# Optimization experiments

Hardware: AMD Instinct MI355X
Metric: run time of the kernel (lower is better)

The kernel has to match this reference:

```python
import jax, jax.numpy as jnp
import numpy as np

VOCAB, B, T, H, E = 32000, 32, 128, 128, 128

def setup_inputs() -> dict:
    key = jax.random.key(0)
    ks = jax.random.split(key, 10)
    s = 0.05
    return {
        "inputs": jax.random.randint(ks[0], (B, T), 0, VOCAB, dtype=jnp.int32),
        "emb": jax.random.normal(ks[1], (VOCAB, E), jnp.float32) * s,
        "W0": jax.random.normal(ks[2], (E, 4 * H), jnp.float32) * s,
        "U0": jax.random.normal(ks[3], (H, 4 * H), jnp.float32) * s,
        "b0": jnp.zeros((4 * H,), jnp.float32),
        "W1": jax.random.normal(ks[4], (H, 4 * H), jnp.float32) * s,
        "U1": jax.random.normal(ks[5], (H, 4 * H), jnp.float32) * s,
        "b1": jnp.zeros((4 * H,), jnp.float32),
        "Wd": jax.random.normal(ks[6], (H, VOCAB), jnp.float32) * s,
        "bd": jnp.zeros((VOCAB,), jnp.float32),
    }

def _lstm_cell(x, h, c, W, U, b):
    # Keras LSTMCell gate order: i, f, c(candidate), o
    z = x @ W + h @ U + b  # [B, 4H]
    zi, zf, zc, zo = jnp.split(z, 4, axis=-1)
    i = jax.nn.sigmoid(zi)
    f = jax.nn.sigmoid(zf)
    o = jax.nn.sigmoid(zo)
    c_new = f * c + i * jnp.tanh(zc)
    h_new = o * jnp.tanh(c_new)
    return h_new, c_new

def reference(inputs, emb, W0, U0, b0, W1, U1, b1, Wd, bd):
    x = emb[inputs]  # [B, T, E]
    xt = jnp.transpose(x, (1, 0, 2))  # [T, B, E]
    zeros = jnp.zeros((x.shape[0], H), x.dtype)
    init = (zeros, zeros, zeros, zeros)  # h0, c0, h1, c1

    def step(carry, x_t):
        h0, c0, h1, c1 = carry
        h0, c0 = _lstm_cell(x_t, h0, c0, W0, U0, b0)
        h1, c1 = _lstm_cell(h0, h1, c1, W1, U1, b1)
        return (h0, c0, h1, c1), h1

    _, ys = jax.lax.scan(step, init, xt)  # ys: [T, B, H]
    y = jnp.transpose(ys, (1, 0, 2))  # [B, T, H]
    logits = y @ Wd + bd  # [B, T, VOCAB]
    return logits
```

## Files before the change

kernel.cpp:

```cpp
#include <hip/hip_runtime.h>
#include <math.h>

#define BB 32
#define TT 128
#define EE 128
#define HD 128
#define G4 512
#define NV 32000

typedef _Float16 f16x2  __attribute__((ext_vector_type(2)));
typedef _Float16 f16x4v __attribute__((ext_vector_type(4)));
typedef _Float16 f16x8  __attribute__((ext_vector_type(8)));
typedef float    f32x4  __attribute__((ext_vector_type(4)));

__global__ __launch_bounds__(256) void k_embed(
    const int* __restrict__ inputs, const float* __restrict__ emb,
    const float* __restrict__ W0, const float* __restrict__ b0,
    float* __restrict__ Z0x)
{
    __shared__ float xs[8][EE];
    const int r0 = blockIdx.x * 8;
    const int tid = threadIdx.x;
    for (int i = tid; i < 8 * EE; i += 256) {
        int r = i >> 7, e = i & 127;
        int tok = inputs[r0 + r];
        xs[r][e] = emb[tok * EE + e];
    }
    __syncthreads();
    const int c2 = tid * 2;
    float2 bb2 = *(const float2*)&b0[c2];
    float acc[8][2];
    #pragma unroll
    for (int r = 0; r < 8; ++r) { acc[r][0] = bb2.x; acc[r][1] = bb2.y; }
    for (int e = 0; e < EE; ++e) {
        float2 w = *(const float2*)&W0[e * G4 + c2];
        #pragma unroll
        for (int r = 0; r < 8; ++r) {
            float x = xs[r][e];
            acc[r][0] = fmaf(x, w.x, acc[r][0]);
            acc[r][1] = fmaf(x, w.y, acc[r][1]);
        }
    }
    #pragma unroll
    for (int r = 0; r < 8; ++r) {
        float2 o2; o2.x = acc[r][0]; o2.y = acc[r][1];
        *(float2*)&Z0x[(size_t)(r0 + r) * G4 + c2] = o2;
    }
}

__device__ __forceinline__ float sigf(float x) {
    return __builtin_amdgcn_rcpf(1.f + __builtin_amdgcn_exp2f(x * -1.44269504088896f));
}
__device__ __forceinline__ float tanh_f(float x) {
    return 1.f - 2.f * __builtin_amdgcn_rcpf(1.f + __builtin_amdgcn_exp2f(x * 2.88539008177793f));
}
__device__ __forceinline__ f16x8 ldfrag(const float* __restrict__ M, int col, int k0) {
    f16x8 v;
    #pragma unroll
    for (int j = 0; j < 8; ++j) v[j] = (_Float16)M[(size_t)(k0 + j) * G4 + col];
    return v;
}

#define REP8(X) X(0) X(1) X(2) X(3) X(4) X(5) X(6) X(7)
#define MFMA(acc, a, b) acc = __builtin_amdgcn_mfma_f32_16x16x32_f16(a, b, acc, 0, 0, 0)

#define DECLF(n) f16x8 u0_##n##_0, u0_##n##_1, u0_##n##_2, u0_##n##_3, \
                       w1_##n##_0, w1_##n##_1, w1_##n##_2, w1_##n##_3, \
                       u1_##n##_0, u1_##n##_1, u1_##n##_2, u1_##n##_3;

#define LOADF(n) { const int cn = wc0 + (n) * 16 + lo16; \
    u0_##n##_0 = ldfrag(U0, cn, khi);      u0_##n##_1 = ldfrag(U0, cn, 32 + khi); \
    u0_##n##_2 = ldfrag(U0, cn, 64 + khi); u0_##n##_3 = ldfrag(U0, cn, 96 + khi); \
    w1_##n##_0 = ldfrag(W1, cn, khi);      w1_##n##_1 = ldfrag(W1, cn, 32 + khi); \
    w1_##n##_2 = ldfrag(W1, cn, 64 + khi); w1_##n##_3 = ldfrag(W1, cn, 96 + khi); \
    asm("" : "+a"(w1_##n##_0), "+a"(w1_##n##_1), "+a"(w1_##n##_2), "+a"(w1_##n##_3)); \
    u1_##n##_0 = ldfrag(U1, cn, khi);      u1_##n##_1 = ldfrag(U1, cn, 32 + khi); \
    u1_##n##_2 = ldfrag(U1, cn, 64 + khi); u1_##n##_3 = ldfrag(U1, cn, 96 + khi); \
    asm("" : "+a"(u1_##n##_0), "+a"(u1_##n##_1), "+a"(u1_##n##_2), "+a"(u1_##n##_3)); }

#define PA(n) { f32x4 acc = {0.f, 0.f, 0.f, 0.f}; \
    MFMA(acc, ha0, u0_##n##_0); MFMA(acc, ha1, u0_##n##_1); \
    MFMA(acc, ha2, u0_##n##_2); MFMA(acc, ha3, u0_##n##_3); \
    if (lane < 32) { const int cw = wc0 + (n) * 16 + lo16; const int br = (lane >> 4) * 4; \
        zbuf[br + 0][cw] = acc[0]; zbuf[br + 1][cw] = acc[1]; \
        zbuf[br + 2][cw] = acc[2]; zbuf[br + 3][cw] = acc[3]; } }

#define PC(n) { f32x4 acc = {0.f, 0.f, 0.f, 0.f}; \
    MFMA(acc, ha0, w1_##n##_0); MFMA(acc, ha1, w1_##n##_1); \
    MFMA(acc, ha2, w1_##n##_2); MFMA(acc, ha3, w1_##n##_3); \
    MFMA(acc, hb0, u1_##n##_0); MFMA(acc, hb1, u1_##n##_1); \
    MFMA(acc, hb2, u1_##n##_2); MFMA(acc, hb3, u1_##n##_3); \
    if (lane < 32) { const int cw = wc0 + (n) * 16 + lo16; const int br = (lane >> 4) * 4; \
        zbuf[br + 0][cw] = acc[0]; zbuf[br + 1][cw] = acc[1]; \
        zbuf[br + 2][cw] = acc[2]; zbuf[br + 3][cw] = acc[3]; } }

#define GT0(K, ZI, ZF, ZC, ZO) { \
    float ig = sigf(ZI), fg = sigf(ZF), og = sigf(ZO), gg = tanh_f(ZC); \
    float cn = fg * c0v[K] + ig * gg; c0v[K] = cn; hv[K] = (_Float16)(og * tanh_f(cn)); }

#define GT1(K, ZI, ZF, ZC, ZO, YO) { \
    float ig = sigf(ZI), fg = sigf(ZF), og = sigf(ZO), gg = tanh_f(ZC); \
    float cn = fg * c1v[K] + ig * gg; c1v[K] = cn; float hn = og * tanh_f(cn); \
    hv[K] = (_Float16)hn; YO = hn; }

__global__ __launch_bounds__(256, 1) void k_lstm_mw(
    const float* __restrict__ Z0x,
    const float* __restrict__ U0, const float* __restrict__ W1,
    const float* __restrict__ U1, const float* __restrict__ b1,
    float* __restrict__ y,
    const float* __restrict__ Wd, _Float16* __restrict__ Whi, _Float16* __restrict__ Wlo)
{
    const int tid  = threadIdx.x;

    if (blockIdx.x >= 4) {
        if (Whi == nullptr) return;
        const int g = (blockIdx.x - 4) * 256 + tid;
        const int chunk = g >> 6;
        const int ln = g & 63;
        const int ntile = chunk >> 2;
        const int kstep = chunk & 3;
        const int n = ntile * 16 + (ln & 15);
        const int kb = kstep * 32 + (ln >> 4) * 8;
        _Float16 hi[8], lo[8];
        #pragma unroll
        for (int j = 0; j < 8; ++j) {
            float v = Wd[(size_t)(kb + j) * NV + n];
            hi[j] = (_Float16)v;
            lo[j] = (_Float16)(v - (float)hi[j]);
        }
        *(float4*)&Whi[(size_t)chunk * 512 + ln * 8] = *(const float4*)hi;
        *(float4*)&Wlo[(size_t)chunk * 512 + ln * 8] = *(const float4*)lo;
        return;
    }

    const int lane = tid & 63;
    const int wc0  = (tid >> 6) * 128;
    const int lo16 = lane & 15;
    const int khi  = (lane >> 4) * 8;
    const int B0   = blockIdx.x * 8;

    __shared__ float     zbuf[8][516];
    __shared__ _Float16  h0p[16][136];
    __shared__ _Float16  h1p[16][136];

    REP8(DECLF)
    REP8(LOADF)

    const int bq  = tid >> 5;
    const int h0i = (tid & 31) * 4;
    const float* zx_base = Z0x + ((size_t)(B0 + bq) * TT) * G4;
    float*       y_base  = y   + ((size_t)(B0 + bq) * TT) * HD + h0i;

    const float4 b1_i = *(const float4*)&b1[0 * 128 + h0i];
    const float4 b1_f = *(const float4*)&b1[1 * 128 + h0i];
    const float4 b1_c = *(const float4*)&b1[2 * 128 + h0i];
    const float4 b1_o = *(const float4*)&b1[3 * 128 + h0i];

    for (int i = tid; i < 16 * 136; i += 256) {
        ((_Float16*)h0p)[i] = (_Float16)0.f;
        ((_Float16*)h1p)[i] = (_Float16)0.f;
    }
    f32x4 c0v = {0.f, 0.f, 0.f, 0.f};
    f32x4 c1v = {0.f, 0.f, 0.f, 0.f};
    __syncthreads();

    for (int t = 0; t < TT; ++t) {
        const float* zx = zx_base + (size_t)t * G4;
        const float4 x_i = *(const float4*)&zx[0 * 128 + h0i];
        const float4 x_f = *(const float4*)&zx[1 * 128 + h0i];
        const float4 x_c = *(const float4*)&zx[2 * 128 + h0i];
        const float4 x_o = *(const float4*)&zx[3 * 128 + h0i];

        {
            f16x8 ha0 = *(const f16x8*)&h0p[lo16][khi];
            f16x8 ha1 = *(const f16x8*)&h0p[lo16][32 + khi];
            f16x8 ha2 = *(const f16x8*)&h0p[lo16][64 + khi];
            f16x8 ha3 = *(const f16x8*)&h0p[lo16][96 + khi];
            REP8(PA)
        }
        __syncthreads();

        {
            const float4 zi4 = *(const float4*)&zbuf[bq][0 * 128 + h0i];
            const float4 zf4 = *(const float4*)&zbuf[bq][1 * 128 + h0i];
            const float4 zc4 = *(const float4*)&zbuf[bq][2 * 128 + h0i];
            const float4 zo4 = *(const float4*)&zbuf[bq][3 * 128 + h0i];
            f16x4v hv;
            GT0(0, zi4.x + x_i.x, zf4.x + x_f.x, zc4.x + x_c.x, zo4.x + x_o.x)
            GT0(1, zi4.y + x_i.y, zf4.y + x_f.y, zc4.y + x_c.y, zo4.y + x_o.y)
            GT0(2, zi4.z + x_i.z, zf4.z + x_f.z, zc4.z + x_c.z, zo4.z + x_o.z)
            GT0(3, zi4.w + x_i.w, zf4.w + x_f.w, zc4.w + x_c.w, zo4.w + x_o.w)
            *(f16x4v*)&h0p[bq][h0i] = hv;
        }
        __syncthreads();

        {
            f16x8 ha0 = *(const f16x8*)&h0p[lo16][khi];
            f16x8 ha1 = *(const f16x8*)&h0p[lo16][32 + khi];
            f16x8 ha2 = *(const f16x8*)&h0p[lo16][64 + khi];
            f16x8 ha3 = *(const f16x8*)&h0p[lo16][96 + khi];
            f16x8 hb0 = *(const f16x8*)&h1p[lo16][khi];
            f16x8 hb1 = *(const f16x8*)&h1p[lo16][32 + khi];
            f16x8 hb2 = *(const f16x8*)&h1p[lo16][64 + khi];
            f16x8 hb3 = *(const f16x8*)&h1p[lo16][96 + khi];
            REP8(PC)
        }
        __syncthreads();

        {
            const float4 zi4 = *(const float4*)&zbuf[bq][0 * 128 + h0i];
            const float4 zf4 = *(const float4*)&zbuf[bq][1 * 128 + h0i];
            const float4 zc4 = *(const float4*)&zbuf[bq][2 * 128 + h0i];
            const float4 zo4 = *(const float4*)&zbuf[bq][3 * 128 + h0i];
            f16x4v hv; float4 yv;
            GT1(0, zi4.x + b1_i.x, zf4.x + b1_f.x, zc4.x + b1_c.x, zo4.x + b1_o.x, yv.x)
            GT1(1, zi4.y + b1_i.y, zf4.y + b1_f.y, zc4.y + b1_c.y, zo4.y + b1_o.y, yv.y)
            GT1(2, zi4.z + b1_i.z, zf4.z + b1_f.z, zc4.z + b1_c.z, zo4.z + b1_o.z, yv.z)
            GT1(3, zi4.w + b1_i.w, zf4.w + b1_f.w, zc4.w + b1_c.w, zo4.w + b1_o.w, yv.w)
            *(f16x4v*)&h1p[bq][h0i] = hv;
            *(float4*)(y_base + (size_t)t * HD) = yv;
        }
        __syncthreads();
    }
}

__global__ __launch_bounds__(256) void k_ysplit(
    const float* __restrict__ y, _Float16* __restrict__ yhi, _Float16* __restrict__ ylo)
{
    const int g = blockIdx.x * 256 + threadIdx.x;
    const int chunk = g >> 6;
    const int lane = g & 63;
    const int mtile = chunk >> 2;
    const int kstep = chunk & 3;
    const int row = mtile * 16 + (lane & 15);
    const int kb = kstep * 32 + (lane >> 4) * 8;
    _Float16 hi[8], lo[8];
    #pragma unroll
    for (int j = 0; j < 8; ++j) {
        float v = y[(size_t)row * HD + kb + j];
        hi[j] = (_Float16)v;
        lo[j] = (_Float16)(v - (float)hi[j]);
    }
    *(float4*)&yhi[(size_t)chunk * 512 + lane * 8] = *(const float4*)hi;
    *(float4*)&ylo[(size_t)chunk * 512 + lane * 8] = *(const float4*)lo;
}

__global__ __launch_bounds__(256) void k_dense_mfma2(
    const _Float16* __restrict__ yhi, const _Float16* __restrict__ ylo,
    const _Float16* __restrict__ Whi, const _Float16* __restrict__ Wlo,
    const float* __restrict__ bd, float* __restrict__ out)
{
    const int tid  = threadIdx.x;
    const int w    = tid >> 6;
    const int lane = tid & 63;
    const int nt0  = blockIdx.y * 16 + w * 4;
    const int mt0  = blockIdx.x * 32;

    f16x8 Bh[4][4], Bl[4][4];
    #pragma unroll
    for (int n = 0; n < 4; ++n) {
        const size_t cb = (size_t)(nt0 + n) * 4 * 512 + lane * 8;
        #pragma unroll
        for (int k = 0; k < 4; ++k) {
            Bh[n][k] = *(const f16x8*)&Whi[cb + k * 512];
            Bl[n][k] = *(const f16x8*)&Wlo[cb + k * 512];
        }
    }
    float bias[4];
    #pragma unroll
    for (int n = 0; n < 4; ++n) bias[n] = bd[(nt0 + n) * 16 + (lane & 15)];

    const int r0 = (lane >> 4) * 4;

    for (int mt = 0; mt < 32; ++mt) {
        const int mtile = mt0 + mt;
        const size_t ab = (size_t)mtile * 4 * 512 + lane * 8;

        f32x4 acc0[4] = {{0,0,0,0},{0,0,0,0},{0,0,0,0},{0,0,0,0}};
        f32x4 acc1[4] = {{0,0,0,0},{0,0,0,0},{0,0,0,0},{0,0,0,0}};

        {
            f16x8 A0 = *(const f16x8*)&yhi[ab];
            f16x8 A1 = *(const f16x8*)&yhi[ab + 512];
            f16x8 A2 = *(const f16x8*)&yhi[ab + 1024];
            f16x8 A3 = *(const f16x8*)&yhi[ab + 1536];
            #pragma unroll
            for (int n = 0; n < 4; ++n) {
                acc0[n] = __builtin_amdgcn_mfma_f32_16x16x32_f16(A0, Bh[n][0], acc0[n], 0, 0, 0);
                acc0[n] = __builtin_amdgcn_mfma_f32_16x16x32_f16(A1, Bh[n][1], acc0[n], 0, 0, 0);
                acc0[n] = __builtin_amdgcn_mfma_f32_16x16x32_f16(A2, Bh[n][2], acc0[n], 0, 0, 0);
                acc0[n] = __builtin_amdgcn_mfma_f32_16x16x32_f16(A3, Bh[n][3], acc0[n], 0, 0, 0);
                acc1[n] = __builtin_amdgcn_mfma_f32_16x16x32_f16(A0, Bl[n][0], acc1[n], 0, 0, 0);
                acc1[n] = __builtin_amdgcn_mfma_f32_16x16x32_f16(A1, Bl[n][1], acc1[n], 0, 0, 0);
                acc1[n] = __builtin_amdgcn_mfma_f32_16x16x32_f16(A2, Bl[n][2], acc1[n], 0, 0, 0);
                acc1[n] = __builtin_amdgcn_mfma_f32_16x16x32_f16(A3, Bl[n][3], acc1[n], 0, 0, 0);
            }
        }
        {
            f16x8 A0 = *(const f16x8*)&ylo[ab];
            f16x8 A1 = *(const f16x8*)&ylo[ab + 512];
            f16x8 A2 = *(const f16x8*)&ylo[ab + 1024];
            f16x8 A3 = *(const f16x8*)&ylo[ab + 1536];
            #pragma unroll
            for (int n = 0; n < 4; ++n) {
                acc1[n] = __builtin_amdgcn_mfma_f32_16x16x32_f16(A0, Bh[n][0], acc1[n], 0, 0, 0);
                acc1[n] = __builtin_amdgcn_mfma_f32_16x16x32_f16(A1, Bh[n][1], acc1[n], 0, 0, 0);
                acc1[n] = __builtin_amdgcn_mfma_f32_16x16x32_f16(A2, Bh[n][2], acc1[n], 0, 0, 0);
                acc1[n] = __builtin_amdgcn_mfma_f32_16x16x32_f16(A3, Bh[n][3], acc1[n], 0, 0, 0);
            }
        }
        const int m0 = mtile * 16;
        #pragma unroll
        for (int n = 0; n < 4; ++n) {
            const int col = (nt0 + n) * 16 + (lane & 15);
            #pragma unroll
            for (int reg = 0; reg < 4; ++reg) {
                out[(size_t)(m0 + r0 + reg) * NV + col] = acc0[n][reg] + acc1[n][reg] + bias[n];
            }
        }
    }
}

__global__ __launch_bounds__(256) void k_dense(
    const float* __restrict__ y, const float* __restrict__ Wd,
    const float* __restrict__ bd, float* __restrict__ out)
{
    __shared__ float ys[64 * HD];
    const int r0 = blockIdx.x * 64;
    const int v0 = blockIdx.y * 128;
    const int tid = threadIdx.x;
    for (int idx = tid; idx < 64 * HD; idx += 256) ys[idx] = y[(size_t)r0 * HD + idx];
    __syncthreads();
    const int tx = tid & 31;
    const int ty = tid >> 5;
    const int v = v0 + tx * 4;
    float4 bd4 = *(const float4*)&bd[v];
    float acc[8][4] = {};
    const float* yrow = &ys[(ty * 8) * HD];
    #pragma unroll 4
    for (int e = 0; e < HD; ++e) {
        float4 wv = *(const float4*)&Wd[(size_t)e * NV + v];
        #pragma unroll
        for (int j = 0; j < 8; ++j) {
            float yv = yrow[j * HD + e];
            acc[j][0] = fmaf(yv, wv.x, acc[j][0]);
            acc[j][1] = fmaf(yv, wv.y, acc[j][1]);
            acc[j][2] = fmaf(yv, wv.z, acc[j][2]);
            acc[j][3] = fmaf(yv, wv.w, acc[j][3]);
        }
    }
    #pragma unroll
    for (int j = 0; j < 8; ++j) {
        int rr = r0 + ty * 8 + j;
        float4 o4;
        o4.x = acc[j][0] + bd4.x;
        o4.y = acc[j][1] + bd4.y;
        o4.z = acc[j][2] + bd4.z;
        o4.w = acc[j][3] + bd4.w;
        *(float4*)&out[(size_t)rr * NV + v] = o4;
    }
}

extern "C" void kernel_launch(void* const* d_in, const int* in_sizes, int n_in,
                              void* d_out, int out_size, void* d_ws, size_t ws_size,
                              hipStream_t stream)
{
    const int*   inputs = (const int*)  d_in[0];
    const float* emb    = (const float*)d_in[1];
    const float* W0     = (const float*)d_in[2];
    const float* U0     = (const float*)d_in[3];
    const float* b0     = (const float*)d_in[4];
    const float* W1     = (const float*)d_in[5];
    const float* U1     = (const float*)d_in[6];
    const float* b1     = (const float*)d_in[7];
    const float* Wd     = (const float*)d_in[8];
    const float* bd     = (const float*)d_in[9];
    float* out = (float*)d_out;

    const size_t Z0X_B = (size_t)8 * 1024 * 1024;
    const size_t YY_B  = (size_t)2 * 1024 * 1024;
    const size_t WSP_B = (size_t)8000 * 512 * 2;
    const size_t YSP_B = (size_t)1024 * 512 * 2;
    const size_t NEED  = Z0X_B + YY_B + 2 * WSP_B + 2 * YSP_B + 4096;

    char* ws = (char*)d_ws;

    if (ws_size >= NEED) {
        float*     Z0x = (float*)ws;
        float*     yy  = (float*)(ws + Z0X_B);
        _Float16*  Whi = (_Float16*)(ws + Z0X_B + YY_B);
        _Float16*  Wlo = (_Float16*)(ws + Z0X_B + YY_B + WSP_B);
        _Float16*  yhi = (_Float16*)(ws + Z0X_B + YY_B + 2 * WSP_B);
        _Float16*  ylo = (_Float16*)(ws + Z0X_B + YY_B + 2 * WSP_B + YSP_B);

        k_embed<<<512, 256, 0, stream>>>(inputs, emb, W0, b0, Z0x);
        k_lstm_mw<<<2004, 256, 0, stream>>>(Z0x, U0, W1, U1, b1, yy, Wd, Whi, Wlo);
        k_ysplit<<<256, 256, 0, stream>>>(yy, yhi, ylo);
        k_dense_mfma2<<<dim3(8, 125), 256, 0, stream>>>(yhi, ylo, Whi, Wlo, bd, out);
    } else {
        float* yy = (float*)ws;
        size_t out_bytes = (size_t)out_size * sizeof(float);
        float* Z0x = (float*)((char*)d_out + out_bytes - Z0X_B);

        k_embed<<<512, 256, 0, stream>>>(inputs, emb, W0, b0, Z0x);
        k_lstm_mw<<<2004, 256, 0, stream>>>(Z0x, U0, W1, U1, b1, yy,
                                            Wd, nullptr, nullptr);
        k_dense<<<dim3(64, 250), 256, 0, stream>>>(yy, Wd, bd, out);
    }
}
```

Baseline: 549.6 us.

## Split LSTM recurrence across eight waves per block instead of four

The recurrent LSTM kernel now runs 512 threads (8 waves) per batch group, and each wave owns 64 gate columns instead of 128. This halves the register-resident weight fragments and the MFMA chain per wave, and spreads gate math over twice as many threads (2 hidden units each). The goal is to shorten the serial per-timestep critical path, at the cost of more waves taking part in each block barrier. The Wd-split side blocks are adjusted to the larger block size with half as many blocks.

```diff
diff --git a/kernel.cpp b/kernel.cpp
--- a/kernel.cpp
+++ b/kernel.cpp
@@ -61,14 +61,14 @@
     return v;
 }
 
-#define REP8(X) X(0) X(1) X(2) X(3) X(4) X(5) X(6) X(7)
+#define REP4(X) X(0) X(1) X(2) X(3)
 #define MFMA(acc, a, b) acc = __builtin_amdgcn_mfma_f32_16x16x32_f16(a, b, acc, 0, 0, 0)
 
 #define DECLF(n) f16x8 u0_##n##_0, u0_##n##_1, u0_##n##_2, u0_##n##_3, \
                        w1_##n##_0, w1_##n##_1, w1_##n##_2, w1_##n##_3, \
                        u1_##n##_0, u1_##n##_1, u1_##n##_2, u1_##n##_3;
 
-#define LOADF(n) { const int cn = wc0 + (n) * 16 + lo16; \
+#define LOADF(n) { const int cn = wu0 + (n) * 16 + lo16; \
     u0_##n##_0 = ldfrag(U0, cn, khi);      u0_##n##_1 = ldfrag(U0, cn, 32 + khi); \
     u0_##n##_2 = ldfrag(U0, cn, 64 + khi); u0_##n##_3 = ldfrag(U0, cn, 96 + khi); \
     w1_##n##_0 = ldfrag(W1, cn, khi);      w1_##n##_1 = ldfrag(W1, cn, 32 + khi); \
@@ -81,7 +81,7 @@
 #define PA(n) { f32x4 acc = {0.f, 0.f, 0.f, 0.f}; \
     MFMA(acc, ha0, u0_##n##_0); MFMA(acc, ha1, u0_##n##_1); \
     MFMA(acc, ha2, u0_##n##_2); MFMA(acc, ha3, u0_##n##_3); \
-    if (lane < 32) { const int cw = wc0 + (n) * 16 + lo16; const int br = (lane >> 4) * 4; \
+    if (lane < 32) { const int cw = wu0 + (n) * 16 + lo16; const int br = (lane >> 4) * 4; \
         zbuf[br + 0][cw] = acc[0]; zbuf[br + 1][cw] = acc[1]; \
         zbuf[br + 2][cw] = acc[2]; zbuf[br + 3][cw] = acc[3]; } }
 
@@ -90,20 +90,19 @@
     MFMA(acc, ha2, w1_##n##_2); MFMA(acc, ha3, w1_##n##_3); \
     MFMA(acc, hb0, u1_##n##_0); MFMA(acc, hb1, u1_##n##_1); \
     MFMA(acc, hb2, u1_##n##_2); MFMA(acc, hb3, u1_##n##_3); \
-    if (lane < 32) { const int cw = wc0 + (n) * 16 + lo16; const int br = (lane >> 4) * 4; \
+    if (lane < 32) { const int cw = wu0 + (n) * 16 + lo16; const int br = (lane >> 4) * 4; \
         zbuf[br + 0][cw] = acc[0]; zbuf[br + 1][cw] = acc[1]; \
         zbuf[br + 2][cw] = acc[2]; zbuf[br + 3][cw] = acc[3]; } }
 
-#define GT0(K, ZI, ZF, ZC, ZO) { \
+#define GT0C(C, ZI, ZF, ZC, ZO) { \
     float ig = sigf(ZI), fg = sigf(ZF), og = sigf(ZO), gg = tanh_f(ZC); \
-    float cn = fg * c0v[K] + ig * gg; c0v[K] = cn; hv[K] = (_Float16)(og * tanh_f(cn)); }
-
-#define GT1(K, ZI, ZF, ZC, ZO, YO) { \
+    float cn = fg * c0v.C + ig * gg; c0v.C = cn; hv.C = og * tanh_f(cn); }
+
+#define GT1C(C, ZI, ZF, ZC, ZO) { \
     float ig = sigf(ZI), fg = sigf(ZF), og = sigf(ZO), gg = tanh_f(ZC); \
-    float cn = fg * c1v[K] + ig * gg; c1v[K] = cn; float hn = og * tanh_f(cn); \
-    hv[K] = (_Float16)hn; YO = hn; }
-
-__global__ __launch_bounds__(256, 1) void k_lstm_mw(
+    float cn = fg * c1v.C + ig * gg; c1v.C = cn; hv.C = og * tanh_f(cn); }
+
+__global__ __launch_bounds__(512, 2) void k_lstm_w8(
     const float* __restrict__ Z0x,
     const float* __restrict__ U0, const float* __restrict__ W1,
     const float* __restrict__ U1, const float* __restrict__ b1,
@@ -114,7 +113,7 @@
 
     if (blockIdx.x >= 4) {
         if (Whi == nullptr) return;
-        const int g = (blockIdx.x - 4) * 256 + tid;
+        const int g = (blockIdx.x - 4) * 512 + tid;
         const int chunk = g >> 6;
         const int ln = g & 63;
         const int ntile = chunk >> 2;
@@ -134,7 +133,7 @@
     }
 
     const int lane = tid & 63;
-    const int wc0  = (tid >> 6) * 128;
+    const int wu0  = (tid >> 6) * 64;
     const int lo16 = lane & 15;
     const int khi  = (lane >> 4) * 8;
     const int B0   = blockIdx.x * 8;
@@ -143,54 +142,53 @@
     __shared__ _Float16  h0p[16][136];
     __shared__ _Float16  h1p[16][136];
 
-    REP8(DECLF)
-    REP8(LOADF)
-
-    const int bq  = tid >> 5;
-    const int h0i = (tid & 31) * 4;
+    REP4(DECLF)
+    REP4(LOADF)
+
+    const int bq  = tid >> 6;
+    const int h0i = (tid & 63) * 2;
     const float* zx_base = Z0x + ((size_t)(B0 + bq) * TT) * G4;
     float*       y_base  = y   + ((size_t)(B0 + bq) * TT) * HD + h0i;
 
-    const float4 b1_i = *(const float4*)&b1[0 * 128 + h0i];
-    const float4 b1_f = *(const float4*)&b1[1 * 128 + h0i];
-    const float4 b1_c = *(const float4*)&b1[2 * 128 + h0i];
-    const float4 b1_o = *(const float4*)&b1[3 * 128 + h0i];
-
-    for (int i = tid; i < 16 * 136; i += 256) {
+    const float2 b1_i = *(const float2*)&b1[0 * 128 + h0i];
+    const float2 b1_f = *(const float2*)&b1[1 * 128 + h0i];
+    const float2 b1_c = *(const float2*)&b1[2 * 128 + h0i];
+    const float2 b1_o = *(const float2*)&b1[3 * 128 + h0i];
+
+    for (int i = tid; i < 16 * 136; i += 512) {
         ((_Float16*)h0p)[i] = (_Float16)0.f;
         ((_Float16*)h1p)[i] = (_Float16)0.f;
     }
-    f32x4 c0v = {0.f, 0.f, 0.f, 0.f};
-    f32x4 c1v = {0.f, 0.f, 0.f, 0.f};
+    float2 c0v = {0.f, 0.f};
+    float2 c1v = {0.f, 0.f};
     __syncthreads();
 
     for (int t = 0; t < TT; ++t) {
         const float* zx = zx_base + (size_t)t * G4;
-        const float4 x_i = *(const float4*)&zx[0 * 128 + h0i];
-        const float4 x_f = *(const float4*)&zx[1 * 128 + h0i];
-        const float4 x_c = *(const float4*)&zx[2 * 128 + h0i];
-        const float4 x_o = *(const float4*)&zx[3 * 128 + h0i];
+        const float2 x_i = *(const float2*)&zx[0 * 128 + h0i];
+        const float2 x_f = *(const float2*)&zx[1 * 128 + h0i];
+        const float2 x_c = *(const float2*)&zx[2 * 128 + h0i];
+        const float2 x_o = *(const float2*)&zx[3 * 128 + h0i];
 
         {
             f16x8 ha0 = *(const f16x8*)&h0p[lo16][khi];
             f16x8 ha1 = *(const f16x8*)&h0p[lo16][32 + khi];
             f16x8 ha2 = *(const f16x8*)&h0p[lo16][64 + khi];
             f16x8 ha3 = *(const f16x8*)&h0p[lo16][96 + khi];
-            REP8(PA)
+            REP4(PA)
         }
         __syncthreads();
 
         {
-            const float4 zi4 = *(const float4*)&zbuf[bq][0 * 128 + h0i];
-            const float4 zf4 = *(const float4*)&zbuf[bq][1 * 128 + h0i];
-            const float4 zc4 = *(const float4*)&zbuf[bq][2 * 128 + h0i];
-            const float4 zo4 = *(const float4*)&zbuf[bq][3 * 128 + h0i];
-            f16x4v hv;
-            GT0(0, zi4.x + x_i.x, zf4.x + x_f.x, zc4.x + x_c.x, zo4.x + x_o.x)
-            GT0(1, zi4.y + x_i.y, zf4.y + x_f.y, zc4.y + x_c.y, zo4.y + x_o.y)
-            GT0(2, zi4.z + x_i.z, zf4.z + x_f.z, zc4.z + x_c.z, zo4.z + x_o.z)
-            GT0(3, zi4.w + x_i.w, zf4.w + x_f.w, zc4.w + x_c.w, zo4.w + x_o.w)
-            *(f16x4v*)&h0p[bq][h0i] = hv;
+            const float2 zi2 = *(const float2*)&zbuf[bq][0 * 128 + h0i];
+            const float2 zf2 = *(const float2*)&zbuf[bq][1 * 128 + h0i];
+            const float2 zc2 = *(const float2*)&zbuf[bq][2 * 128 + h0i];
+            const float2 zo2 = *(const float2*)&zbuf[bq][3 * 128 + h0i];
+            float2 hv;
+            GT0C(x, zi2.x + x_i.x, zf2.x + x_f.x, zc2.x + x_c.x, zo2.x + x_o.x)
+            GT0C(y, zi2.y + x_i.y, zf2.y + x_f.y, zc2.y + x_c.y, zo2.y + x_o.y)
+            f16x2 hp; hp[0] = (_Float16)hv.x; hp[1] = (_Float16)hv.y;
+            *(f16x2*)&h0p[bq][h0i] = hp;
         }
         __syncthreads();
 
@@ -203,22 +201,21 @@
             f16x8 hb1 = *(const f16x8*)&h1p[lo16][32 + khi];
             f16x8 hb2 = *(const f16x8*)&h1p[lo16][64 + khi];
             f16x8 hb3 = *(const f16x8*)&h1p[lo16][96 + khi];
-            REP8(PC)
+            REP4(PC)
         }
         __syncthreads();
 
         {
-            const float4 zi4 = *(const float4*)&zbuf[bq][0 * 128 + h0i];
-            const float4 zf4 = *(const float4*)&zbuf[bq][1 * 128 + h0i];
-            const float4 zc4 = *(const float4*)&zbuf[bq][2 * 128 + h0i];
-            const float4 zo4 = *(const float4*)&zbuf[bq][3 * 128 + h0i];
-            f16x4v hv; float4 yv;
-            GT1(0, zi4.x + b1_i.x, zf4.x + b1_f.x, zc4.x + b1_c.x, zo4.x + b1_o.x, yv.x)
-            GT1(1, zi4.y + b1_i.y, zf4.y + b1_f.y, zc4.y + b1_c.y, zo4.y + b1_o.y, yv.y)
-            GT1(2, zi4.z + b1_i.z, zf4.z + b1_f.z, zc4.z + b1_c.z, zo4.z + b1_o.z, yv.z)
-            GT1(3, zi4.w + b1_i.w, zf4.w + b1_f.w, zc4.w + b1_c.w, zo4.w + b1_o.w, yv.w)
-            *(f16x4v*)&h1p[bq][h0i] = hv;
-            *(float4*)(y_base + (size_t)t * HD) = yv;
+            const float2 zi2 = *(const float2*)&zbuf[bq][0 * 128 + h0i];
+            const float2 zf2 = *(const float2*)&zbuf[bq][1 * 128 + h0i];
+            const float2 zc2 = *(const float2*)&zbuf[bq][2 * 128 + h0i];
+            const float2 zo2 = *(const float2*)&zbuf[bq][3 * 128 + h0i];
+            float2 hv;
+            GT1C(x, zi2.x + b1_i.x, zf2.x + b1_f.x, zc2.x + b1_c.x, zo2.x + b1_o.x)
+            GT1C(y, zi2.y + b1_i.y, zf2.y + b1_f.y, zc2.y + b1_c.y, zo2.y + b1_o.y)
+            f16x2 hp; hp[0] = (_Float16)hv.x; hp[1] = (_Float16)hv.y;
+            *(f16x2*)&h1p[bq][h0i] = hp;
+            *(float2*)(y_base + (size_t)t * HD) = hv;
         }
         __syncthreads();
     }
@@ -394,7 +391,7 @@
         _Float16*  ylo = (_Float16*)(ws + Z0X_B + YY_B + 2 * WSP_B + YSP_B);
 
         k_embed<<<512, 256, 0, stream>>>(inputs, emb, W0, b0, Z0x);
-        k_lstm_mw<<<2004, 256, 0, stream>>>(Z0x, U0, W1, U1, b1, yy, Wd, Whi, Wlo);
+        k_lstm_w8<<<1004, 512, 0, stream>>>(Z0x, U0, W1, U1, b1, yy, Wd, Whi, Wlo);
         k_ysplit<<<256, 256, 0, stream>>>(yy, yhi, ylo);
         k_dense_mfma2<<<dim3(8, 125), 256, 0, stream>>>(yhi, ylo, Whi, Wlo, bd, out);
     } else {
@@ -403,7 +400,7 @@
         float* Z0x = (float*)((char*)d_out + out_bytes - Z0X_B);
 
         k_embed<<<512, 256, 0, stream>>>(inputs, emb, W0, b0, Z0x);
-        k_lstm_mw<<<2004, 256, 0, stream>>>(Z0x, U0, W1, U1, b1, yy,
+        k_lstm_w8<<<1004, 512, 0, stream>>>(Z0x, U0, W1, U1, b1, yy,
                                             Wd, nullptr, nullptr);
         k_dense<<<dim3(64, 250), 256, 0, stream>>>(yy, Wd, bd, out);
     }
```

Result: no change. 559.3 us (+1.8%).
